# Performance work log

Measured on AMD Instinct MI355X. Metric: run time of the kernel, lower is better.

The kernel has to match this reference:

```python
import jax, jax.numpy as jnp
import numpy as np
from jax import lax

NQ = 4      # num_qubits
DEPTH = 2
DIM = 2 ** NQ  # 16

def _maxpool2(x):
    # MaxPool2d(kernel_size=2, stride=1), NCHW
    return lax.reduce_window(x, -jnp.inf, lax.max, (1, 1, 2, 2), (1, 1, 1, 1), 'VALID')

def _conv(x, w, b, stride, pad):
    y = lax.conv_general_dilated(x, w, (stride, stride), [(pad, pad), (pad, pad)],
                                 dimension_numbers=('NCHW', 'OIHW', 'NCHW'))
    return y + b[None, :, None, None]

def _apply_1q(state, gate, q):
    # state: (B, 16) complex64; gate: (2,2) shared or (B,2,2) per-sample. wire 0 = MSB.
    B = state.shape[0]
    s = state.reshape(B, 2 ** q, 2, 2 ** (NQ - 1 - q))
    sub = 'ij,bljr->blir' if gate.ndim == 2 else 'bij,bljr->blir'
    return jnp.einsum(sub, gate, s).reshape(B, DIM)

def _quantum_head(angles, weights):
    # Batched statevector simulation of: RX(angles[i]) encoding, then DEPTH x
    # [RY(w) on every wire, CZ chain], then <Z_0>, <Z_1>.
    B = angles.shape[0]
    state = jnp.zeros((B, DIM), jnp.complex64).at[:, 0].set(1.0)
    for q in range(NQ):  # RX encoding (per-sample angles)
        t = angles[:, q] * 0.5
        c = jnp.cos(t).astype(jnp.complex64)
        s = (-1j) * jnp.sin(t).astype(jnp.complex64)
        gate = jnp.stack([jnp.stack([c, s], -1), jnp.stack([s, c], -1)], -2)  # (B,2,2)
        state = _apply_1q(state, gate, q)
    idxs = jnp.arange(DIM)
    w_idx = 0
    for _ in range(DEPTH):
        for q in range(NQ):  # RY(weights) shared across batch
            t = weights[w_idx] * 0.5
            w_idx += 1
            c, s = jnp.cos(t), jnp.sin(t)
            gate = jnp.stack([jnp.stack([c, -s]), jnp.stack([s, c])]).astype(jnp.complex64)
            state = _apply_1q(state, gate, q)
        for q in range(NQ - 1):  # CZ(q, q+1): -1 phase where both bits set
            both = ((idxs >> (NQ - 1 - q)) & 1) & ((idxs >> (NQ - 2 - q)) & 1)
            phase = jnp.where(both == 1, -1.0, 1.0).astype(jnp.complex64)
            state = state * phase[None, :]
    probs = state.real ** 2 + state.imag ** 2  # (B,16) float32
    logits = []
    for q in range(2):  # expval PauliZ on wires 0,1
        sign = 1.0 - 2.0 * ((idxs >> (NQ - 1 - q)) & 1).astype(jnp.float32)
        logits.append(probs @ sign)
    return jnp.stack(logits, -1)  # (B,2)


def setup_inputs() -> dict:
    key = jax.random.key(0)
    ks = jax.random.split(key, 12)
    x = jax.random.normal(ks[0], (256, 3, 250, 250), jnp.float32)
    w1 = jax.random.normal(ks[1], (6, 3, 5, 5), jnp.float32) * 0.05
    b1 = jnp.zeros((6,), jnp.float32)
    w2 = jax.random.normal(ks[2], (15, 6, 3, 3), jnp.float32) * 0.05
    b2 = jnp.zeros((15,), jnp.float32)
    fc1_w = jax.random.normal(ks[3], (120, 55815), jnp.float32) * 0.004
    fc1_b = jnp.zeros((120,), jnp.float32)
    fc2_w = jax.random.normal(ks[4], (84, 120), jnp.float32) * 0.09
    fc2_b = jnp.zeros((84,), jnp.float32)
    fc3_w = jax.random.normal(ks[5], (4, 84), jnp.float32) * 0.1
    fc3_b = jnp.zeros((4,), jnp.float32)
    qweights = jax.random.normal(ks[6], (NQ * DEPTH,), jnp.float32)
    return {'x': x, 'w1': w1, 'b1': b1, 'w2': w2, 'b2': b2,
            'fc1_w': fc1_w, 'fc1_b': fc1_b, 'fc2_w': fc2_w, 'fc2_b': fc2_b,
            'fc3_w': fc3_w, 'fc3_b': fc3_b, 'qweights': qweights}


def reference(x, w1, b1, w2, b2, fc1_w, fc1_b, fc2_w, fc2_b, fc3_w, fc3_b, qweights):
    # Dropout layers act as identity (eval mode).
    h = jax.nn.relu(_conv(x, w1, b1, stride=2, pad=1))   # (B,6,124,124)
    h = _maxpool2(h)                                      # (B,6,123,123)
    h = jax.nn.relu(_conv(h, w2, b2, stride=2, pad=1))   # (B,15,62,62)
    h = _maxpool2(h)                                      # (B,15,61,61)
    h = h.reshape(h.shape[0], -1)                         # (B,55815)
    h = jax.nn.relu(h @ fc1_w.T + fc1_b)
    h = jax.nn.relu(h @ fc2_w.T + fc2_b)
    angles = h @ fc3_w.T + fc3_b                          # (B,4)
    logits = _quantum_head(angles, qweights)              # (B,2)
    return jax.nn.softmax(logits, axis=-1)
```

## Files before the change

kernel.cpp:

```cpp
#include <hip/hip_runtime.h>
#include <hip/hip_bf16.h>
#include <hip/hip_fp16.h>
#include <math.h>

#define B 256
#define FC1_K   55815
#define FC1_N   120
#define FC2_N   84
#define KP        57344
#define FC1_SPLIT 256
#define FC1_KC    (KP / FC1_SPLIT)

typedef __attribute__((ext_vector_type(8))) short bf16x8;
typedef __attribute__((ext_vector_type(4))) float f32x4;
typedef _Float16 half2_t __attribute__((ext_vector_type(2)));

static __device__ __forceinline__ unsigned short bf16_bits(float f) {
    __hip_bfloat16 h = __float2bfloat16(f);
    return *(unsigned short*)&h;
}
static __device__ __forceinline__ unsigned short f16_bits(float f) {
    __half h = __float2half(f);
    return *(unsigned short*)&h;
}
static __device__ __forceinline__ half2_t h2_from_u32(unsigned int u) {
    return __builtin_bit_cast(half2_t, u);
}

#define ASYNC_CP(g, l) __builtin_amdgcn_global_load_lds( \
    (const __attribute__((address_space(1))) void*)(g),  \
    (__attribute__((address_space(3))) void*)(l), 4, 0, 0)

__global__ __launch_bounds__(256) void prep_kernel(
    const float* __restrict__ fc1_w, const float* __restrict__ w2,
    unsigned short* __restrict__ wb, unsigned int* __restrict__ w2pk,
    float* __restrict__ zeros) {
    const int n = blockIdx.y;
    const int k0 = blockIdx.x * 2048 + threadIdx.x * 8;
    bf16x8 v8;
    #pragma unroll
    for (int i = 0; i < 8; ++i) v8[i] = 0;
    if (n < FC1_N) {
        const float* src = fc1_w + (size_t)n * FC1_K + k0;
        if (k0 + 8 <= FC1_K) {
            #pragma unroll
            for (int i = 0; i < 8; ++i) v8[i] = (short)bf16_bits(src[i]);
        } else {
            #pragma unroll
            for (int i = 0; i < 8; ++i)
                if (k0 + i < FC1_K) v8[i] = (short)bf16_bits(src[i]);
        }
    }
    *(bf16x8*)(wb + (size_t)n * KP + k0) = v8;

    if (blockIdx.x == 0 && n == 0) {
        int t = threadIdx.x;
        if (t < 64) zeros[t] = 0.f;
        for (int f = t; f < 540; f += 256) {
            int pr = f & 1, g = f >> 1;
            int o = g % 15, r = g / 15, ky = r % 3, c = r / 3;
            const float* wsrc = w2 + (o * 6 + c) * 9 + ky * 3;
            unsigned int pk;
            if (pr == 0) pk = (unsigned)f16_bits(wsrc[0]) | ((unsigned)f16_bits(wsrc[1]) << 16);
            else         pk = (unsigned)f16_bits(wsrc[2]);
            w2pk[((c * 3 + ky) * 15 + o) * 2 + pr] = pk;
        }
    }
}

#define C1_ROW 276
__global__ __launch_bounds__(256) void conv1_pool1_kernel(
    const float* __restrict__ x, const float* __restrict__ w1,
    const float* __restrict__ b1, unsigned short* __restrict__ pool1,
    const float* __restrict__ zeros) {
    __shared__ __align__(16) float in_t[2][19 * C1_ROW];
    unsigned short* out_t = (unsigned short*)&in_t[1][0];

    const int tid = threadIdx.x;
    const int wave = tid >> 6, lane = tid & 63;
    const int PB = 7 * blockIdx.x;
    const int b  = blockIdx.y;
    const int cg = tid & 31, rr = tid >> 5;
    const int iyb = 2 * PB - 1;

    const int g0 = cg >> 3, o0 = 8 * (cg & 7);
    const int a0 = g0 * 68 + o0;
    const int a2 = (o0 < 56) ? (a0 + 8) : ((g0 + 1) * 68);

    float acc[4][6];
    #pragma unroll
    for (int j = 0; j < 4; ++j)
        #pragma unroll
        for (int o = 0; o < 6; ++o) acc[j][o] = b1[o];

    {
        const float* xp = x + (size_t)(b * 3 + 0) * 62500;
        #pragma unroll
        for (int i = 0; i < 19; ++i) {
            int chunk = wave * 19 + i;
            int row = chunk >> 2, g = chunk & 3;
            int iy = iyb + row, col = g * 64 + lane - 1;
            const float* gp = ((unsigned)iy < 250u && (unsigned)col < 250u)
                              ? (xp + iy * 250 + col) : zeros;
            ASYNC_CP(gp, &in_t[0][row * C1_ROW + g * 68]);
        }
    }
    __syncthreads();
    for (int c = 0; c < 3; ++c) {
        if (c < 2) {
            const float* xp = x + (size_t)(b * 3 + c + 1) * 62500;
            float* dstb = &in_t[(c + 1) & 1][0];
            #pragma unroll
            for (int i = 0; i < 19; ++i) {
                int chunk = wave * 19 + i;
                int row = chunk >> 2, g = chunk & 3;
                int iy = iyb + row, col = g * 64 + lane - 1;
                const float* gp = ((unsigned)iy < 250u && (unsigned)col < 250u)
                                  ? (xp + iy * 250 + col) : zeros;
                ASYNC_CP(gp, dstb + row * C1_ROW + g * 68);
            }
        }
        const float* bufp = &in_t[c & 1][0];
        #pragma unroll
        for (int ky = 0; ky < 5; ++ky) {
            const float* rowp = bufp + (2 * rr + ky) * C1_ROW;
            float f[12];
            float4 v0 = *(const float4*)(rowp + a0);
            float4 v1 = *(const float4*)(rowp + a0 + 4);
            float4 v2 = *(const float4*)(rowp + a2);
            f[0]=v0.x; f[1]=v0.y; f[2]=v0.z; f[3]=v0.w;
            f[4]=v1.x; f[5]=v1.y; f[6]=v1.z; f[7]=v1.w;
            f[8]=v2.x; f[9]=v2.y; f[10]=v2.z; f[11]=v2.w;
            #pragma unroll
            for (int kx = 0; kx < 5; ++kx) {
                #pragma unroll
                for (int j = 0; j < 4; ++j) {
                    float xv = f[2 * j + kx];
                    #pragma unroll
                    for (int o = 0; o < 6; ++o)
                        acc[j][o] += xv * w1[(o * 3 + c) * 25 + ky * 5 + kx];
                }
            }
        }
        if (c < 2) __syncthreads();
    }
    #pragma unroll
    for (int o = 0; o < 6; ++o) {
        unsigned short h0 = f16_bits(fmaxf(acc[0][o], 0.f));
        unsigned short h1 = f16_bits(fmaxf(acc[1][o], 0.f));
        unsigned short h2 = f16_bits(fmaxf(acc[2][o], 0.f));
        unsigned short h3 = f16_bits(fmaxf(acc[3][o], 0.f));
        uint2 pk;
        pk.x = (unsigned)h0 | ((unsigned)h1 << 16);
        pk.y = (unsigned)h2 | ((unsigned)h3 << 16);
        *(uint2*)&out_t[(o * 8 + rr) * 132 + 4 * cg] = pk;
    }
    __syncthreads();
    for (int it = tid; it < 6 * 7 * 32; it += 256) {
        int g = it & 31, rem = it >> 5;
        int pyl = rem % 7, oc = rem / 7;
        int py = PB + pyl;
        if (py >= 123) continue;
        const unsigned short* q0 = &out_t[(oc * 8 + pyl) * 132 + 4 * g];
        const unsigned short* q1 = q0 + 132;
        uint2 ua = *(const uint2*)q0;
        uint2 ub = *(const uint2*)q1;
        unsigned short va[5] = {(unsigned short)(ua.x & 0xffff), (unsigned short)(ua.x >> 16),
                                (unsigned short)(ua.y & 0xffff), (unsigned short)(ua.y >> 16), q0[4]};
        unsigned short vb[5] = {(unsigned short)(ub.x & 0xffff), (unsigned short)(ub.x >> 16),
                                (unsigned short)(ub.y & 0xffff), (unsigned short)(ub.y >> 16), q1[4]};
        unsigned short* dst = pool1 + ((size_t)(b * 6 + oc) * 123 + py) * 128;
        #pragma unroll
        for (int j = 0; j < 4; ++j) {
            int px = 4 * g + j;
            if (px >= 127) continue;
            unsigned short m = 0;
            if (px <= 122) {
                unsigned short m0 = va[j] > va[j+1] ? va[j] : va[j+1];
                unsigned short m1 = vb[j] > vb[j+1] ? vb[j] : vb[j+1];
                m = m0 > m1 ? m0 : m1;
            }
            dst[1 + px] = m;
        }
        if (g == 0) dst[0] = 0;
    }
}

__global__ __launch_bounds__(128) void conv2_pool2_kernel(
    const unsigned short* __restrict__ pool1, const unsigned int* __restrict__ w2pk,
    const float* __restrict__ b2, unsigned short* __restrict__ A) {
    __shared__ __align__(16) unsigned int in2[2][17 * 64];
    __shared__ __align__(16) unsigned short out2[15 * 8 * 68];

    const int tid = threadIdx.x;
    const int wave = tid >> 6, lane = tid & 63;
    const int PB = 7 * blockIdx.x;
    const int b  = blockIdx.y;
    const int cg = tid & 15, rr = tid >> 4;
    const int iyb = 2 * PB - 1;

    float acc[4][15];
    #pragma unroll
    for (int j = 0; j < 4; ++j)
        #pragma unroll
        for (int o = 0; o < 15; ++o) acc[j][o] = b2[o];

    const unsigned int* p1u = (const unsigned int*)pool1;

    {
        const unsigned int* pp = p1u + (size_t)(b * 6 + 0) * (123 * 64);
        #pragma unroll
        for (int i = 0; i < 9; ++i) {
            int chunk = wave * 9 + i;
            if (chunk < 17) {
                int iy = iyb + chunk;
                if ((unsigned)iy < 123u) ASYNC_CP(pp + iy * 64 + lane, &in2[0][chunk * 64]);
                else                     in2[0][chunk * 64 + lane] = 0;
            }
        }
    }
    __syncthreads();
    for (int c = 0; c < 6; ++c) {
        if (c < 5) {
            const unsigned int* pp = p1u + (size_t)(b * 6 + c + 1) * (123 * 64);
            unsigned int* dstb = &in2[(c + 1) & 1][0];
            #pragma unroll
            for (int i = 0; i < 9; ++i) {
                int chunk = wave * 9 + i;
                if (chunk < 17) {
                    int iy = iyb + chunk;
                    if ((unsigned)iy < 123u) ASYNC_CP(pp + iy * 64 + lane, dstb + chunk * 64);
                    else                     dstb[chunk * 64 + lane] = 0;
                }
            }
        }
        const unsigned int* bufp = &in2[c & 1][0];
        #pragma unroll
        for (int ky = 0; ky < 3; ++ky) {
            const unsigned int* rp = bufp + (2 * rr + ky) * 64 + 4 * cg;
            half2_t dd[5];
            {
                uint4 u4 = *(const uint4*)rp;
                unsigned int u5 = rp[4];
                dd[0] = h2_from_u32(u4.x); dd[1] = h2_from_u32(u4.y);
                dd[2] = h2_from_u32(u4.z); dd[3] = h2_from_u32(u4.w);
                dd[4] = h2_from_u32(u5);
            }
            const unsigned int* wrow = w2pk + (c * 3 + ky) * 30;
            #pragma unroll
            for (int j = 0; j < 4; ++j) {
                #pragma unroll
                for (int o = 0; o < 15; ++o) {
                    acc[j][o] = __builtin_amdgcn_fdot2(dd[j],     h2_from_u32(wrow[o * 2]),
                                                       acc[j][o], false);
                    acc[j][o] = __builtin_amdgcn_fdot2(dd[j + 1], h2_from_u32(wrow[o * 2 + 1]),
                                                       acc[j][o], false);
                }
            }
        }
        if (c < 5) __syncthreads();
    }
    #pragma unroll
    for (int o = 0; o < 15; ++o) {
        unsigned short h0 = bf16_bits(fmaxf(acc[0][o], 0.f));
        unsigned short h1 = bf16_bits(fmaxf(acc[1][o], 0.f));
        unsigned short h2 = bf16_bits(fmaxf(acc[2][o], 0.f));
        unsigned short h3 = bf16_bits(fmaxf(acc[3][o], 0.f));
        uint2 pk;
        pk.x = (unsigned)h0 | ((unsigned)h1 << 16);
        pk.y = (unsigned)h2 | ((unsigned)h3 << 16);
        *(uint2*)&out2[(o * 8 + rr) * 68 + 4 * cg] = pk;
    }
    __syncthreads();
    for (int it = tid; it < 15 * 7 * 16; it += 128) {
        int g = it & 15, rem = it >> 4;
        int pyl = rem % 7, oc = rem / 7;
        int py = PB + pyl;
        if (py >= 61) continue;
        const unsigned short* q0 = &out2[(oc * 8 + pyl) * 68 + 4 * g];
        const unsigned short* q1 = q0 + 68;
        uint2 ua = *(const uint2*)q0;
        uint2 ub = *(const uint2*)q1;
        unsigned short va[5] = {(unsigned short)(ua.x & 0xffff), (unsigned short)(ua.x >> 16),
                                (unsigned short)(ua.y & 0xffff), (unsigned short)(ua.y >> 16), q0[4]};
        unsigned short vb[5] = {(unsigned short)(ub.x & 0xffff), (unsigned short)(ub.x >> 16),
                                (unsigned short)(ub.y & 0xffff), (unsigned short)(ub.y >> 16), q1[4]};
        #pragma unroll
        for (int j = 0; j < 4; ++j) {
            int px = 4 * g + j;
            if (px < 61) {
                unsigned short m0 = va[j] > va[j+1] ? va[j] : va[j+1];
                unsigned short m1 = vb[j] > vb[j+1] ? vb[j] : vb[j+1];
                unsigned short m = m0 > m1 ? m0 : m1;
                A[(size_t)b * KP + (oc * 61 + py) * 61 + px] = m;
            }
        }
    }
}

__global__ __launch_bounds__(256) void fc1_mfma_kernel(
    const __hip_bfloat16* __restrict__ A, const __hip_bfloat16* __restrict__ W,
    float* __restrict__ partial) {
    const int wave = threadIdx.x >> 6, lane = threadIdx.x & 63;
    const int mrow = lane & 15, quad = lane >> 4;
    const int m0 = blockIdx.x * 128 + wave * 32;
    const int k0 = blockIdx.y * FC1_KC;

    f32x4 acc[2][8];
    #pragma unroll
    for (int i = 0; i < 2; ++i)
        #pragma unroll
        for (int j = 0; j < 8; ++j) acc[i][j] = (f32x4){0.f, 0.f, 0.f, 0.f};

    const short* Ap = (const short*)A;
    const short* Wp = (const short*)W;
    for (int ks = 0; ks < FC1_KC; ks += 32) {
        const int kk = k0 + ks + quad * 8;
        const bf16x8 a0 = *(const bf16x8*)(Ap + (size_t)(m0 + mrow) * KP + kk);
        const bf16x8 a1 = *(const bf16x8*)(Ap + (size_t)(m0 + 16 + mrow) * KP + kk);
        #pragma unroll
        for (int nt = 0; nt < 8; ++nt) {
            const bf16x8 bb = *(const bf16x8*)(Wp + (size_t)(nt * 16 + mrow) * KP + kk);
            acc[0][nt] = __builtin_amdgcn_mfma_f32_16x16x32_bf16(a0, bb, acc[0][nt], 0, 0, 0);
            acc[1][nt] = __builtin_amdgcn_mfma_f32_16x16x32_bf16(a1, bb, acc[1][nt], 0, 0, 0);
        }
    }
    float* po = partial + (size_t)blockIdx.y * (256 * 128);
    #pragma unroll
    for (int mt = 0; mt < 2; ++mt)
        #pragma unroll
        for (int nt = 0; nt < 8; ++nt)
            #pragma unroll
            for (int r = 0; r < 4; ++r)
                po[(m0 + mt * 16 + quad * 4 + r) * 128 + nt * 16 + mrow] = acc[mt][nt][r];
}

__global__ __launch_bounds__(512) void tail_kernel(
    const float* __restrict__ partial, const float* __restrict__ fc1_b,
    const float* __restrict__ fc2_w, const float* __restrict__ fc2_b,
    const float* __restrict__ fc3_w, const float* __restrict__ fc3_b,
    const float* __restrict__ qw, float* __restrict__ out) {
    __shared__ float h1p[4][FC1_N];
    __shared__ float h1[FC1_N];
    __shared__ float h2[FC2_N];
    __shared__ float ang[4];
    int b = blockIdx.x;
    int t = threadIdx.x;
    int grp = t >> 7, tt = t & 127;

    if (tt < FC1_N) {
        const float* p = partial + b * 128 + tt;
        float sum = 0.f;
        #pragma unroll 8
        for (int s = grp * 64; s < grp * 64 + 64; ++s) sum += p[(size_t)s * (256 * 128)];
        h1p[grp][tt] = sum;
    }
    __syncthreads();
    if (t < FC1_N)
        h1[t] = fmaxf(h1p[0][t] + h1p[1][t] + h1p[2][t] + h1p[3][t] + fc1_b[t], 0.f);
    __syncthreads();
    if (t < FC2_N) {
        float acc = fc2_b[t];
        const float* w = fc2_w + t * FC1_N;
        for (int k = 0; k < FC1_N; ++k) acc += h1[k] * w[k];
        h2[t] = fmaxf(acc, 0.f);
    }
    __syncthreads();
    if (t < 4) {
        float acc = fc3_b[t];
        const float* w = fc3_w + t * FC2_N;
        for (int k = 0; k < FC2_N; ++k) acc += h2[k] * w[k];
        ang[t] = acc;
    }
    __syncthreads();
    if (t < 16) {
        const int lane = t;
        float sr = (lane == 0) ? 1.f : 0.f, si = 0.f;
        #pragma unroll
        for (int q = 0; q < 4; ++q) {
            float th = ang[q] * 0.5f;
            float c = __cosf(th), s = __sinf(th);
            int mask = 8 >> q;
            float pr = __shfl_xor(sr, mask, 16);
            float pi = __shfl_xor(si, mask, 16);
            float nr = c * sr + s * pi;
            float ni = c * si - s * pr;
            sr = nr; si = ni;
        }
        int widx = 0;
        #pragma unroll
        for (int d = 0; d < 2; ++d) {
            #pragma unroll
            for (int q = 0; q < 4; ++q) {
                float th = qw[widx++] * 0.5f;
                float c = __cosf(th), s = __sinf(th);
                int mask = 8 >> q;
                float pr = __shfl_xor(sr, mask, 16);
                float pi = __shfl_xor(si, mask, 16);
                float sg = (lane & mask) ? s : -s;
                sr = c * sr + sg * pr;
                si = c * si + sg * pi;
            }
            #pragma unroll
            for (int q = 0; q < 3; ++q) {
                int m1 = 8 >> q, m2 = 4 >> q;
                if ((lane & m1) && (lane & m2)) { sr = -sr; si = -si; }
            }
        }
        float p = sr * sr + si * si;
        float v0 = (lane & 8) ? -p : p;
        float v1 = (lane & 4) ? -p : p;
        #pragma unroll
        for (int off = 8; off >= 1; off >>= 1) {
            v0 += __shfl_xor(v0, off, 16);
            v1 += __shfl_xor(v1, off, 16);
        }
        if (lane == 0) {
            float m = fmaxf(v0, v1);
            float e0 = expf(v0 - m), e1 = expf(v1 - m);
            float inv = 1.f / (e0 + e1);
            out[b * 2 + 0] = e0 * inv;
            out[b * 2 + 1] = e1 * inv;
        }
    }
}

extern "C" void kernel_launch(void* const* d_in, const int* in_sizes, int n_in,
                              void* d_out, int out_size, void* d_ws, size_t ws_size,
                              hipStream_t stream) {
    const float* x     = (const float*)d_in[0];
    const float* w1    = (const float*)d_in[1];
    const float* b1    = (const float*)d_in[2];
    const float* w2    = (const float*)d_in[3];
    const float* b2    = (const float*)d_in[4];
    const float* fc1_w = (const float*)d_in[5];
    const float* fc1_b = (const float*)d_in[6];
    const float* fc2_w = (const float*)d_in[7];
    const float* fc2_b = (const float*)d_in[8];
    const float* fc3_w = (const float*)d_in[9];
    const float* fc3_b = (const float*)d_in[10];
    const float* qw    = (const float*)d_in[11];
    float* out = (float*)d_out;

    char* ws = (char*)d_ws;
    const size_t O_POOL1  = 0;
    const size_t O_A      = O_POOL1 + 48365568;
    const size_t O_W      = O_A + 29360128;
    const size_t O_PART   = O_W + 14680064;
    const size_t O_W2PK   = O_PART + 33554432;
    const size_t O_ZERO   = O_W2PK + 4096;
    unsigned short* pool1   = (unsigned short*)(ws + O_POOL1);
    __hip_bfloat16* A_bf16  = (__hip_bfloat16*)(ws + O_A);
    __hip_bfloat16* W_bf16  = (__hip_bfloat16*)(ws + O_W);
    float*          partial = (float*)(ws + O_PART);
    unsigned int*   w2pk    = (unsigned int*)(ws + O_W2PK);
    float*          zeros   = (float*)(ws + O_ZERO);

    prep_kernel<<<dim3(KP / 2048, 128), 256, 0, stream>>>(
        fc1_w, w2, (unsigned short*)W_bf16, w2pk, zeros);
    conv1_pool1_kernel<<<dim3(18, B), 256, 0, stream>>>(x, w1, b1, pool1, zeros);
    conv2_pool2_kernel<<<dim3(9, B), 128, 0, stream>>>(pool1, w2pk, b2,
                                                       (unsigned short*)A_bf16);
    fc1_mfma_kernel<<<dim3(2, FC1_SPLIT), 256, 0, stream>>>(A_bf16, W_bf16, partial);
    tail_kernel<<<B, 512, 0, stream>>>(partial, fc1_b, fc2_w, fc2_b,
                                       fc3_w, fc3_b, qw, out);
}
```

Measured before the change: 461.7 us.

## Compute conv1 with f16 MFMA via im2col gather from LDS

Rewrites conv1 to use 16x16x32 f16 MFMA instructions instead of scalar FMA loops. Weight fragments are pre-packed into f16 in the prep kernel, and each lane gathers 8 taps from the LDS input tile and packs them with round-toward-zero f16 conversion. The LDS input layout drops its per-group padding, and the output tile layout changes to match the MFMA accumulator lanes. This removes the large scalar FMA cost, at the price of wasted MFMA work (6 of 16 output channels used, 25 of 32 taps), extra LDS gathers, and reduced input precision to f16.

```diff
diff --git a/kernel.cpp b/kernel.cpp
--- a/kernel.cpp
+++ b/kernel.cpp
@@ -14,6 +14,7 @@
 typedef __attribute__((ext_vector_type(8))) short bf16x8;
 typedef __attribute__((ext_vector_type(4))) float f32x4;
 typedef _Float16 half2_t __attribute__((ext_vector_type(2)));
+typedef _Float16 f16x8 __attribute__((ext_vector_type(8)));
 
 static __device__ __forceinline__ unsigned short bf16_bits(float f) {
     __hip_bfloat16 h = __float2bfloat16(f);
@@ -26,6 +27,9 @@
 static __device__ __forceinline__ half2_t h2_from_u32(unsigned int u) {
     return __builtin_bit_cast(half2_t, u);
 }
+static __device__ __forceinline__ unsigned int pkrtz(float a, float b) {
+    return __builtin_bit_cast(unsigned int, __builtin_amdgcn_cvt_pkrtz(a, b));
+}
 
 #define ASYNC_CP(g, l) __builtin_amdgcn_global_load_lds( \
     (const __attribute__((address_space(1))) void*)(g),  \
@@ -33,8 +37,9 @@
 
 __global__ __launch_bounds__(256) void prep_kernel(
     const float* __restrict__ fc1_w, const float* __restrict__ w2,
+    const float* __restrict__ w1,
     unsigned short* __restrict__ wb, unsigned int* __restrict__ w2pk,
-    float* __restrict__ zeros) {
+    unsigned short* __restrict__ wfrag, float* __restrict__ zeros) {
     const int n = blockIdx.y;
     const int k0 = blockIdx.x * 2048 + threadIdx.x * 8;
     bf16x8 v8;
@@ -65,33 +70,60 @@
             else         pk = (unsigned)f16_bits(wsrc[2]);
             w2pk[((c * 3 + ky) * 15 + o) * 2 + pr] = pk;
         }
+        for (int f = t; f < 1536; f += 256) {
+            int i = f & 7, ln = (f >> 3) & 63, c = f >> 9;
+            int nn = ln & 15, qq = ln >> 4;
+            int tap = qq * 8 + i;
+            float v = (nn < 6 && tap < 25) ? w1[(nn * 3 + c) * 25 + tap] : 0.f;
+            wfrag[f] = f16_bits(v);
+        }
     }
 }
 
 #define C1_ROW 276
-__global__ __launch_bounds__(256) void conv1_pool1_kernel(
-    const float* __restrict__ x, const float* __restrict__ w1,
+#define C1_BUF (19 * C1_ROW)
+#define OT_RS 136
+#define OT_PS 1104
+__global__ __launch_bounds__(256, 3) void conv1_pool1_kernel(
+    const float* __restrict__ x, const unsigned short* __restrict__ wfrag,
     const float* __restrict__ b1, unsigned short* __restrict__ pool1,
     const float* __restrict__ zeros) {
-    __shared__ __align__(16) float in_t[2][19 * C1_ROW];
+    __shared__ __align__(16) float in_t[2][C1_BUF];
     unsigned short* out_t = (unsigned short*)&in_t[1][0];
 
     const int tid = threadIdx.x;
     const int wave = tid >> 6, lane = tid & 63;
     const int PB = 7 * blockIdx.x;
     const int b  = blockIdx.y;
-    const int cg = tid & 31, rr = tid >> 5;
     const int iyb = 2 * PB - 1;
-
-    const int g0 = cg >> 3, o0 = 8 * (cg & 7);
-    const int a0 = g0 * 68 + o0;
-    const int a2 = (o0 < 56) ? (a0 + 8) : ((g0 + 1) * 68);
-
-    float acc[4][6];
-    #pragma unroll
-    for (int j = 0; j < 4; ++j)
-        #pragma unroll
-        for (int o = 0; o < 6; ++o) acc[j][o] = b1[o];
+    const int m = lane & 15, q = lane >> 4;
+
+    f16x8 bw[3];
+    #pragma unroll
+    for (int c = 0; c < 3; ++c)
+        bw[c] = __builtin_bit_cast(f16x8, *(const uint4*)(wfrag + (c * 64 + lane) * 8));
+
+    const float bias = (m < 6) ? b1[m] : 0.f;
+    f32x4 acc[2][8];
+    #pragma unroll
+    for (int r2 = 0; r2 < 2; ++r2)
+        #pragma unroll
+        for (int tb = 0; tb < 8; ++tb)
+            acc[r2][tb] = (f32x4){bias, bias, bias, bias};
+
+    int addr[2][8];
+    #pragma unroll
+    for (int r2 = 0; r2 < 2; ++r2) {
+        int cr = wave * 2 + r2;
+        #pragma unroll
+        for (int i = 0; i < 8; ++i) {
+            int t = q * 8 + i;
+            t = t > 24 ? 24 : t;
+            int ky = (t * 13) >> 6;
+            int kx = t - 5 * ky;
+            addr[r2][i] = ((2 * cr + ky) * C1_ROW + 2 * m + kx) * 4;
+        }
+    }
 
     {
         const float* xp = x + (size_t)(b * 3 + 0) * 62500;
@@ -102,10 +134,12 @@
             int iy = iyb + row, col = g * 64 + lane - 1;
             const float* gp = ((unsigned)iy < 250u && (unsigned)col < 250u)
                               ? (xp + iy * 250 + col) : zeros;
-            ASYNC_CP(gp, &in_t[0][row * C1_ROW + g * 68]);
-        }
-    }
-    __syncthreads();
+            ASYNC_CP(gp, &in_t[0][row * C1_ROW + g * 64]);
+        }
+    }
+    __syncthreads();
+    const char* ldsb = (const char*)&in_t[0][0];
+    #pragma unroll
     for (int c = 0; c < 3; ++c) {
         if (c < 2) {
             const float* xp = x + (size_t)(b * 3 + c + 1) * 62500;
@@ -117,43 +151,44 @@
                 int iy = iyb + row, col = g * 64 + lane - 1;
                 const float* gp = ((unsigned)iy < 250u && (unsigned)col < 250u)
                                   ? (xp + iy * 250 + col) : zeros;
-                ASYNC_CP(gp, dstb + row * C1_ROW + g * 68);
-            }
-        }
-        const float* bufp = &in_t[c & 1][0];
-        #pragma unroll
-        for (int ky = 0; ky < 5; ++ky) {
-            const float* rowp = bufp + (2 * rr + ky) * C1_ROW;
-            float f[12];
-            float4 v0 = *(const float4*)(rowp + a0);
-            float4 v1 = *(const float4*)(rowp + a0 + 4);
-            float4 v2 = *(const float4*)(rowp + a2);
-            f[0]=v0.x; f[1]=v0.y; f[2]=v0.z; f[3]=v0.w;
-            f[4]=v1.x; f[5]=v1.y; f[6]=v1.z; f[7]=v1.w;
-            f[8]=v2.x; f[9]=v2.y; f[10]=v2.z; f[11]=v2.w;
-            #pragma unroll
-            for (int kx = 0; kx < 5; ++kx) {
+                ASYNC_CP(gp, dstb + row * C1_ROW + g * 64);
+            }
+        }
+        #pragma unroll
+        for (int r2 = 0; r2 < 2; ++r2) {
+            #pragma unroll
+            for (int tb = 0; tb < 8; ++tb) {
+                float f[8];
                 #pragma unroll
-                for (int j = 0; j < 4; ++j) {
-                    float xv = f[2 * j + kx];
-                    #pragma unroll
-                    for (int o = 0; o < 6; ++o)
-                        acc[j][o] += xv * w1[(o * 3 + c) * 25 + ky * 5 + kx];
-                }
+                for (int i = 0; i < 8; ++i)
+                    f[i] = *(const float*)(ldsb + ((c & 1) * (C1_BUF * 4) + tb * 128)
+                                           + addr[r2][i]);
+                uint4 u;
+                u.x = pkrtz(f[0], f[1]); u.y = pkrtz(f[2], f[3]);
+                u.z = pkrtz(f[4], f[5]); u.w = pkrtz(f[6], f[7]);
+                f16x8 af = __builtin_bit_cast(f16x8, u);
+                acc[r2][tb] = __builtin_amdgcn_mfma_f32_16x16x32_f16(
+                                  af, bw[c], acc[r2][tb], 0, 0, 0);
             }
         }
         if (c < 2) __syncthreads();
     }
     #pragma unroll
-    for (int o = 0; o < 6; ++o) {
-        unsigned short h0 = f16_bits(fmaxf(acc[0][o], 0.f));
-        unsigned short h1 = f16_bits(fmaxf(acc[1][o], 0.f));
-        unsigned short h2 = f16_bits(fmaxf(acc[2][o], 0.f));
-        unsigned short h3 = f16_bits(fmaxf(acc[3][o], 0.f));
-        uint2 pk;
-        pk.x = (unsigned)h0 | ((unsigned)h1 << 16);
-        pk.y = (unsigned)h2 | ((unsigned)h3 << 16);
-        *(uint2*)&out_t[(o * 8 + rr) * 132 + 4 * cg] = pk;
+    for (int r2 = 0; r2 < 2; ++r2) {
+        int cr = wave * 2 + r2;
+        #pragma unroll
+        for (int tb = 0; tb < 8; ++tb) {
+            if (m < 6) {
+                f32x4 a = acc[r2][tb];
+                unsigned h0 = f16_bits(fmaxf(a[0], 0.f));
+                unsigned h1 = f16_bits(fmaxf(a[1], 0.f));
+                unsigned h2 = f16_bits(fmaxf(a[2], 0.f));
+                unsigned h3 = f16_bits(fmaxf(a[3], 0.f));
+                int off = m * OT_PS + cr * OT_RS + tb * 16 + q * 4;
+                *(unsigned int*)&out_t[off]     = h0 | (h1 << 16);
+                *(unsigned int*)&out_t[off + 2] = h2 | (h3 << 16);
+            }
+        }
     }
     __syncthreads();
     for (int it = tid; it < 6 * 7 * 32; it += 256) {
@@ -161,8 +196,8 @@
         int pyl = rem % 7, oc = rem / 7;
         int py = PB + pyl;
         if (py >= 123) continue;
-        const unsigned short* q0 = &out_t[(oc * 8 + pyl) * 132 + 4 * g];
-        const unsigned short* q1 = q0 + 132;
+        const unsigned short* q0 = &out_t[oc * OT_PS + pyl * OT_RS + 4 * g];
+        const unsigned short* q1 = q0 + OT_RS;
         uint2 ua = *(const uint2*)q0;
         uint2 ub = *(const uint2*)q1;
         unsigned short va[5] = {(unsigned short)(ua.x & 0xffff), (unsigned short)(ua.x >> 16),
@@ -174,13 +209,13 @@
         for (int j = 0; j < 4; ++j) {
             int px = 4 * g + j;
             if (px >= 127) continue;
-            unsigned short m = 0;
+            unsigned short mm = 0;
             if (px <= 122) {
                 unsigned short m0 = va[j] > va[j+1] ? va[j] : va[j+1];
                 unsigned short m1 = vb[j] > vb[j+1] ? vb[j] : vb[j+1];
-                m = m0 > m1 ? m0 : m1;
-            }
-            dst[1 + px] = m;
+                mm = m0 > m1 ? m0 : m1;
+            }
+            dst[1 + px] = mm;
         }
         if (g == 0) dst[0] = 0;
     }
@@ -448,17 +483,19 @@
     const size_t O_W      = O_A + 29360128;
     const size_t O_PART   = O_W + 14680064;
     const size_t O_W2PK   = O_PART + 33554432;
-    const size_t O_ZERO   = O_W2PK + 4096;
+    const size_t O_WFRAG  = O_W2PK + 4096;
+    const size_t O_ZERO   = O_WFRAG + 4096;
     unsigned short* pool1   = (unsigned short*)(ws + O_POOL1);
     __hip_bfloat16* A_bf16  = (__hip_bfloat16*)(ws + O_A);
     __hip_bfloat16* W_bf16  = (__hip_bfloat16*)(ws + O_W);
     float*          partial = (float*)(ws + O_PART);
     unsigned int*   w2pk    = (unsigned int*)(ws + O_W2PK);
+    unsigned short* wfrag   = (unsigned short*)(ws + O_WFRAG);
     float*          zeros   = (float*)(ws + O_ZERO);
 
     prep_kernel<<<dim3(KP / 2048, 128), 256, 0, stream>>>(
-        fc1_w, w2, (unsigned short*)W_bf16, w2pk, zeros);
-    conv1_pool1_kernel<<<dim3(18, B), 256, 0, stream>>>(x, w1, b1, pool1, zeros);
+        fc1_w, w2, w1, (unsigned short*)W_bf16, w2pk, wfrag, zeros);
+    conv1_pool1_kernel<<<dim3(18, B), 256, 0, stream>>>(x, wfrag, b1, pool1, zeros);
     conv2_pool2_kernel<<<dim3(9, B), 128, 0, stream>>>(pool1, w2pk, b2,
                                                        (unsigned short*)A_bf16);
     fc1_mfma_kernel<<<dim3(2, FC1_SPLIT), 256, 0, stream>>>(A_bf16, W_bf16, partial);
```

Result: no change. 466.9 us (+1.1%).
